# Optimization experiments

Hardware: AMD Instinct MI355X
Metric: run time of the kernel (lower is better)

Reference implementation:

```python
import jax, jax.numpy as jnp
import numpy as np

T, B, I, H = 128, 128, 256, 256  # numHiddenUnits(=seq len), batch, input_size, hidden_size


def setup_inputs() -> dict:
    key = jax.random.key(0)
    ks = jax.random.split(key, 7)
    stdv = 1.0 / np.sqrt(H)
    u = lambda k, shape: jax.random.uniform(k, shape, jnp.float32, -stdv, stdv)
    return {
        "batch_x": jax.random.normal(ks[0], (T, B, I), jnp.float32),
        "initial_state": jax.random.normal(ks[1], (B, H), jnp.float32),
        "initial_state_c": jax.random.normal(ks[2], (B, H), jnp.float32),
        # distinct weights per timestep (one LSTMCell per t), stacked on dim 0
        "W_input": u(ks[3], (T, I, 4 * H)),
        "B_input": u(ks[4], (T, 4 * H)),
        "W_hidden": u(ks[5], (T, H, 4 * H)),
        "B_hidden": u(ks[6], (T, 4 * H)),
    }


def reference(batch_x, initial_state, initial_state_c, W_input, B_input, W_hidden, B_hidden):
    def step(carry, xs):
        h, c = carry
        x_t, Wi, bi, Wh, bh = xs
        gates = x_t @ Wi + bi + h @ Wh + bh  # [B, 4H]
        i_t, f_t, o_t, g_t = jnp.split(gates, 4, axis=1)  # chunk order: i, f, o, c_tilde
        c = jax.nn.sigmoid(f_t) * c + jax.nn.sigmoid(i_t) * jnp.tanh(g_t)
        h = jax.nn.sigmoid(o_t) * jnp.tanh(c)
        return (h, c), h

    (h, c), outputs = jax.lax.scan(
        step, (initial_state, initial_state_c),
        (batch_x, W_input, B_input, W_hidden, B_hidden))
    return outputs, h, c  # outputs: [T, B, H]
```

## Files before the change

### kernel.cpp

```cpp
#include <hip/hip_runtime.h>
#include <hip/hip_bf16.h>
#include <cmath>

#define T_  128
#define B_  128
#define I_  256
#define H_  256
#define G4_ 1024

#define NP1 512
#define NRP 8192

using frag  = __attribute__((ext_vector_type(8))) short;
using f32x4 = __attribute__((ext_vector_type(4))) float;
using u32x4 = __attribute__((ext_vector_type(4))) unsigned int;

__device__ __forceinline__ unsigned short bf16u(float f) {
    __hip_bfloat16 b = __float2bfloat16(f);
    return __builtin_bit_cast(unsigned short, b);
}

#define BARRIER_SEQ() do {                                   \
    __builtin_amdgcn_sched_barrier(0);                       \
    asm volatile("s_waitcnt lgkmcnt(0)" ::: "memory");       \
    __builtin_amdgcn_s_barrier();                            \
    __builtin_amdgcn_sched_barrier(0);                       \
} while (0)

__global__ __launch_bounds__(512)
void lstm_pre(const float* __restrict__ x, const float* __restrict__ Wi,
              const float* __restrict__ bi, const float* __restrict__ bh,
              const float* __restrict__ Wh,
              float* __restrict__ Gxp, unsigned short* __restrict__ Whp)
{
    const int bid = blockIdx.x;
    const int tid = threadIdx.x;

    if (bid >= NP1) {
        const int pbid = bid - NP1;
        const int tt   = pbid >> 6;
        const int j64  = pbid & 63;
        const int gid  = tt * 32768 + j64 * 512 + tid;
        const int lane = gid & 63;
        const int nb   = (gid >> 6) & 63;
        const int kb   = (gid >> 12) & 7;
        const int k0   = kb * 32 + (lane >> 4) * 8;
        const int col  = nb * 16 + (lane & 15);
        const float* src = Wh + (size_t)(tt * I_ + k0) * G4_ + col;
        unsigned short v[8];
        #pragma unroll
        for (int j = 0; j < 8; ++j) v[j] = bf16u(src[(size_t)j * G4_]);
        uint4 o;
        o.x = v[0] | ((unsigned)v[1] << 16);
        o.y = v[2] | ((unsigned)v[3] << 16);
        o.z = v[4] | ((unsigned)v[5] << 16);
        o.w = v[6] | ((unsigned)v[7] << 16);
        *(uint4*)(Whp + (size_t)gid * 8) = o;
        return;
    }

    __shared__ unsigned short ws[2][16][64][8];

    const int t    = bid >> 2;
    const int q    = bid & 3;
    const int wv   = tid >> 6;
    const int lane = tid & 63;
    const int lrow = lane & 15;
    const int lhi  = lane >> 4;

    frag af[8];
    #pragma unroll
    for (int kb = 0; kb < 8; ++kb) {
        const float* ap = x + ((size_t)(t * B_ + wv * 16 + lrow) * I_ + kb * 32 + lhi * 8);
        float4 f0 = *(const float4*)ap;
        float4 f1 = *(const float4*)(ap + 4);
        u32x4 p;
        p.x = bf16u(f0.x) | ((unsigned)bf16u(f0.y) << 16);
        p.y = bf16u(f0.z) | ((unsigned)bf16u(f0.w) << 16);
        p.z = bf16u(f1.x) | ((unsigned)bf16u(f1.y) << 16);
        p.w = bf16u(f1.z) | ((unsigned)bf16u(f1.w) << 16);
        af[kb] = __builtin_bit_cast(frag, p);
    }

    f32x4 acc[16];
    #pragma unroll
    for (int n = 0; n < 16; ++n) {
        const int gc = (q * 16 + n) * 16 + lrow;
        const float b = bi[(size_t)t * G4_ + gc] + bh[(size_t)t * G4_ + gc];
        acc[n] = (f32x4){b, b, b, b};
    }

    auto stage = [&](int kb, int b) {
        #pragma unroll
        for (int p = 0; p < 2; ++p) {
            const int task = p * 512 + tid;
            const int colL = task & 255;
            const int khi  = task >> 8;
            const float* src = Wi + ((size_t)(t * I_ + kb * 32 + khi * 8) * G4_
                                     + q * 256 + colL);
            unsigned short v[8];
            #pragma unroll
            for (int j = 0; j < 8; ++j) v[j] = bf16u(src[(size_t)j * G4_]);
            uint4 o;
            o.x = v[0] | ((unsigned)v[1] << 16);
            o.y = v[2] | ((unsigned)v[3] << 16);
            o.z = v[4] | ((unsigned)v[5] << 16);
            o.w = v[6] | ((unsigned)v[7] << 16);
            const int nbh = colL >> 4;
            const int lw  = (colL & 15) | (khi << 4);
            *(uint4*)&ws[b][nbh][lw][0] = o;
        }
    };

    stage(0, 0);
    __syncthreads();
    for (int kb = 0; kb < 8; ++kb) {
        if (kb < 7) stage(kb + 1, (kb + 1) & 1);
        #pragma unroll
        for (int n = 0; n < 16; ++n) {
            frag bf = *(const frag*)&ws[kb & 1][n][lane][0];
            acc[n] = __builtin_amdgcn_mfma_f32_16x16x32_bf16(af[kb], bf, acc[n], 0, 0, 0);
        }
        __syncthreads();
    }

    #pragma unroll
    for (int n = 0; n < 16; ++n)
        *(f32x4*)&Gxp[(((size_t)t * 8 + wv) * 64 + q * 16 + n) * 256 + lane * 4] = acc[n];
}

__global__ __launch_bounds__(512, 1)
void lstm_rec(const float* __restrict__ h0, const float* __restrict__ c0in,
              const unsigned short* __restrict__ Whp,
              const float* __restrict__ Gxp, float* __restrict__ out,
              unsigned int* __restrict__ pub)
{
    __shared__ unsigned short h2[2][16][272];
    __shared__ float red[4][4][256];

    const int tid  = threadIdx.x;
    const int wv   = tid >> 6;
    const int lane = tid & 63;
    const int rg   = blockIdx.x & 7;
    const int sl   = blockIdx.x >> 3;
    const int r0   = rg * 16;
    const int oc0  = sl * 64;
    const int lrow = lane & 15;
    const int lhi  = lane >> 4;

    const int kh = wv >> 2;
    const int cb = wv & 3;

    {
        int row = tid >> 5;
        int cc  = (tid & 31) * 8;
        #pragma unroll
        for (int j = 0; j < 8; ++j)
            h2[0][row][cc + j] = bf16u(h0[(size_t)(r0 + row) * H_ + cc + j]);
    }

    float cst[4] = {0.f, 0.f, 0.f, 0.f};
    if (kh == 0) {
        #pragma unroll
        for (int rgi = 0; rgi < 4; ++rgi)
            cst[rgi] = c0in[(size_t)(r0 + lhi * 4 + rgi) * H_ + oc0 + cb * 16 + lrow];
    }

    int prow[12], pcol[12];
    if (kh == 1) {
        const int ltid = tid - 256;
        #pragma unroll
        for (int k = 0; k < 12; ++k) {
            int w  = ltid + k * 256;
            int rr = w / 192;
            int fc = w - rr * 192;
            prow[k] = rr;
            pcol[k] = fc + (fc >= oc0 ? 64 : 0);
        }
    }

    const unsigned short* wl = Whp + (size_t)lane * 8;
    const float*          gl = Gxp + (size_t)lane * 4;

    frag br[4][4];
    #pragma unroll
    for (int kbl = 0; kbl < 4; ++kbl)
        #pragma unroll
        for (int g = 0; g < 4; ++g)
            br[kbl][g] = *(const frag*)(wl +
                (size_t)((kh * 4 + kbl) * 64 + g * 16 + sl * 4 + cb) * 512);

    f32x4 gxr[4];
    if (kh == 0) {
        #pragma unroll
        for (int g = 0; g < 4; ++g)
            gxr[g] = *(const f32x4*)(gl +
                (size_t)((size_t)rg * 64 + g * 16 + sl * 4 + cb) * 256);
    }

    __syncthreads();

    for (int t = 0; t < T_; ++t) {
        f32x4 acc[4];
        if (kh == 0) {
            #pragma unroll
            for (int g = 0; g < 4; ++g) acc[g] = gxr[g];
            if (t + 1 < T_) {
                #pragma unroll
                for (int g = 0; g < 4; ++g)
                    gxr[g] = *(const f32x4*)(gl +
                        (size_t)(((t + 1) * 8 + rg) * 64 + g * 16 + sl * 4 + cb) * 256);
            }
        } else {
            #pragma unroll
            for (int g = 0; g < 4; ++g) acc[g] = (f32x4){0.f, 0.f, 0.f, 0.f};
        }

        #pragma unroll
        for (int kbl = 0; kbl < 4; ++kbl) {
            const int kb = kh * 4 + kbl;
            frag a = *(const frag*)&h2[t & 1][lrow][kb * 32 + lhi * 8];
            #pragma unroll
            for (int g = 0; g < 4; ++g)
                acc[g] = __builtin_amdgcn_mfma_f32_16x16x32_bf16(
                    a, br[kbl][g], acc[g], 0, 0, 0);
            if (t + 1 < T_) {
                #pragma unroll
                for (int g = 0; g < 4; ++g)
                    br[kbl][g] = *(const frag*)(wl +
                        (size_t)(((t + 1) * 8 + kb) * 64 + g * 16 + sl * 4 + cb) * 512);
            }
        }

        if (kh == 1) {
            #pragma unroll
            for (int g = 0; g < 4; ++g)
                *(f32x4*)&red[cb][g][lane * 4] = acc[g];
        }

        BARRIER_SEQ();

        if (kh == 0) {
            #pragma unroll
            for (int g = 0; g < 4; ++g)
                acc[g] += *(const f32x4*)&red[cb][g][lane * 4];
            const int colb = oc0 + cb * 16 + lrow;
            float hv[4];
            unsigned short hb[4];
            #pragma unroll
            for (int rgi = 0; rgi < 4; ++rgi) {
                float gi = acc[0][rgi], gf = acc[1][rgi];
                float go = acc[2][rgi], gg = acc[3][rgi];
                float i_ = __builtin_amdgcn_rcpf(1.f + __expf(-gi));
                float f_ = __builtin_amdgcn_rcpf(1.f + __expf(-gf));
                float o_ = __builtin_amdgcn_rcpf(1.f + __expf(-go));
                float gt = 1.f - 2.f * __builtin_amdgcn_rcpf(__expf(2.f * gg) + 1.f);
                float c  = f_ * cst[rgi] + i_ * gt;
                cst[rgi] = c;
                float tc = 1.f - 2.f * __builtin_amdgcn_rcpf(__expf(2.f * c) + 1.f);
                float h  = o_ * tc;
                hv[rgi] = h;
                hb[rgi] = bf16u(h);
            }
            if (t + 1 < T_) {
                #pragma unroll
                for (int rgi = 0; rgi < 4; ++rgi)
                    __hip_atomic_store(&pub[(size_t)(r0 + lhi * 4 + rgi) * H_ + colb],
                                       ((unsigned)(t + 1) << 16) | hb[rgi],
                                       __ATOMIC_RELAXED, __HIP_MEMORY_SCOPE_AGENT);
            }
            #pragma unroll
            for (int rgi = 0; rgi < 4; ++rgi) {
                const int row = lhi * 4 + rgi;
                out[(size_t)(t * B_ + r0 + row) * H_ + colb] = hv[rgi];
                h2[(t + 1) & 1][row][colb] = hb[rgi];
            }
            if (t == T_ - 1) {
                #pragma unroll
                for (int rgi = 0; rgi < 4; ++rgi) {
                    const int row = lhi * 4 + rgi;
                    out[(size_t)T_ * B_ * H_ + (size_t)(r0 + row) * H_ + colb] = hv[rgi];
                    out[(size_t)T_ * B_ * H_ + B_ * H_ + (size_t)(r0 + row) * H_ + colb] = cst[rgi];
                }
            }
        } else if (t + 1 < T_) {
            const unsigned want = (unsigned)(t + 1);
            while (true) {
                unsigned vv[12];
                #pragma unroll
                for (int k = 0; k < 12; ++k)
                    vv[k] = __hip_atomic_load(
                        &pub[(size_t)(r0 + prow[k]) * H_ + pcol[k]],
                        __ATOMIC_RELAXED, __HIP_MEMORY_SCOPE_AGENT);
                unsigned miss = 0;
                #pragma unroll
                for (int k = 0; k < 12; ++k) {
                    if ((vv[k] >> 16) == want)
                        h2[(t + 1) & 1][prow[k]][pcol[k]] =
                            (unsigned short)(vv[k] & 0xFFFFu);
                    else
                        miss = 1u;
                }
                if (!__any((int)miss)) break;
            }
        }

        BARRIER_SEQ();
    }
}

extern "C" void kernel_launch(void* const* d_in, const int* in_sizes, int n_in,
                              void* d_out, int out_size, void* d_ws, size_t ws_size,
                              hipStream_t stream) {
    const float* x  = (const float*)d_in[0];
    const float* h0 = (const float*)d_in[1];
    const float* c0 = (const float*)d_in[2];
    const float* Wi = (const float*)d_in[3];
    const float* bi = (const float*)d_in[4];
    const float* Wh = (const float*)d_in[5];
    const float* bh = (const float*)d_in[6];
    float* out = (float*)d_out;

    float*          Gxp = (float*)d_ws;
    unsigned short* Whp = (unsigned short*)((char*)d_ws + 67108864);
    unsigned int*   pub = (unsigned int*)((char*)d_ws + 134217728);

    hipMemsetAsync(pub, 0, 131072, stream);
    lstm_pre<<<dim3(NP1 + NRP), dim3(512), 0, stream>>>(x, Wi, bi, bh, Wh, Gxp, Whp);
    lstm_rec<<<dim3(32), dim3(512), 0, stream>>>(h0, c0, Whp, Gxp, out, pub);
}
```

Baseline: 485.8 us.

## Split LSTM gate epilogue and peer polling across both K-half wave groups

Both K-half wave groups now write partial gate sums to shared memory. Each group reduces and computes the LSTM cell update for two of the four rows per lane, instead of one group doing all four while the other only polls. Polling of peer-published hidden values is also split evenly across all 512 threads, and the first poll load is issued before the gate math so its latency overlaps the compute. The aim is to shorten the serial epilogue and cross-block sync on the recurrent critical path, at the cost of more LDS traffic for the reduction buffer.

After: 507.7 us. +4.5%, slower.

```diff
diff --git a/kernel.cpp b/kernel.cpp
--- a/kernel.cpp
+++ b/kernel.cpp
@@ -42,8 +42,8 @@
         const int j64  = pbid & 63;
         const int gid  = tt * 32768 + j64 * 512 + tid;
         const int lane = gid & 63;
+        const int kb   = (gid >> 12) & 7;
         const int nb   = (gid >> 6) & 63;
-        const int kb   = (gid >> 12) & 7;
         const int k0   = kb * 32 + (lane >> 4) * 8;
         const int col  = nb * 16 + (lane & 15);
         const float* src = Wh + (size_t)(tt * I_ + k0) * G4_ + col;
@@ -136,7 +136,7 @@
               unsigned int* __restrict__ pub)
 {
     __shared__ unsigned short h2[2][16][272];
-    __shared__ float red[4][4][256];
+    __shared__ float red[2][4][4][256];
 
     const int tid  = threadIdx.x;
     const int wv   = tid >> 6;
@@ -159,24 +159,20 @@
             h2[0][row][cc + j] = bf16u(h0[(size_t)(r0 + row) * H_ + cc + j]);
     }
 
-    float cst[4] = {0.f, 0.f, 0.f, 0.f};
-    if (kh == 0) {
-        #pragma unroll
-        for (int rgi = 0; rgi < 4; ++rgi)
-            cst[rgi] = c0in[(size_t)(r0 + lhi * 4 + rgi) * H_ + oc0 + cb * 16 + lrow];
-    }
-
-    int prow[12], pcol[12];
-    if (kh == 1) {
-        const int ltid = tid - 256;
-        #pragma unroll
-        for (int k = 0; k < 12; ++k) {
-            int w  = ltid + k * 256;
-            int rr = w / 192;
-            int fc = w - rr * 192;
-            prow[k] = rr;
-            pcol[k] = fc + (fc >= oc0 ? 64 : 0);
-        }
+    const int colb = oc0 + cb * 16 + lrow;
+    float cst[2];
+    #pragma unroll
+    for (int j = 0; j < 2; ++j)
+        cst[j] = c0in[(size_t)(r0 + lhi * 4 + kh * 2 + j) * H_ + colb];
+
+    int prow[6], pcol[6];
+    #pragma unroll
+    for (int k = 0; k < 6; ++k) {
+        int w  = tid + k * 512;
+        int rr = w / 192;
+        int fc = w - rr * 192;
+        prow[k] = rr;
+        pcol[k] = fc + (fc >= oc0 ? 64 : 0);
     }
 
     const unsigned short* wl = Whp + (size_t)lane * 8;
@@ -232,69 +228,77 @@
             }
         }
 
-        if (kh == 1) {
-            #pragma unroll
-            for (int g = 0; g < 4; ++g)
-                *(f32x4*)&red[cb][g][lane * 4] = acc[g];
-        }
+        #pragma unroll
+        for (int g = 0; g < 4; ++g)
+            *(f32x4*)&red[kh][cb][g][lane * 4] = acc[g];
 
         BARRIER_SEQ();
 
-        if (kh == 0) {
-            #pragma unroll
-            for (int g = 0; g < 4; ++g)
-                acc[g] += *(const f32x4*)&red[cb][g][lane * 4];
-            const int colb = oc0 + cb * 16 + lrow;
-            float hv[4];
-            unsigned short hb[4];
-            #pragma unroll
-            for (int rgi = 0; rgi < 4; ++rgi) {
-                float gi = acc[0][rgi], gf = acc[1][rgi];
-                float go = acc[2][rgi], gg = acc[3][rgi];
-                float i_ = __builtin_amdgcn_rcpf(1.f + __expf(-gi));
-                float f_ = __builtin_amdgcn_rcpf(1.f + __expf(-gf));
-                float o_ = __builtin_amdgcn_rcpf(1.f + __expf(-go));
-                float gt = 1.f - 2.f * __builtin_amdgcn_rcpf(__expf(2.f * gg) + 1.f);
-                float c  = f_ * cst[rgi] + i_ * gt;
-                cst[rgi] = c;
-                float tc = 1.f - 2.f * __builtin_amdgcn_rcpf(__expf(2.f * c) + 1.f);
-                float h  = o_ * tc;
-                hv[rgi] = h;
-                hb[rgi] = bf16u(h);
-            }
-            if (t + 1 < T_) {
-                #pragma unroll
-                for (int rgi = 0; rgi < 4; ++rgi)
-                    __hip_atomic_store(&pub[(size_t)(r0 + lhi * 4 + rgi) * H_ + colb],
-                                       ((unsigned)(t + 1) << 16) | hb[rgi],
-                                       __ATOMIC_RELAXED, __HIP_MEMORY_SCOPE_AGENT);
-            }
-            #pragma unroll
-            for (int rgi = 0; rgi < 4; ++rgi) {
-                const int row = lhi * 4 + rgi;
-                out[(size_t)(t * B_ + r0 + row) * H_ + colb] = hv[rgi];
-                h2[(t + 1) & 1][row][colb] = hb[rgi];
-            }
-            if (t == T_ - 1) {
-                #pragma unroll
-                for (int rgi = 0; rgi < 4; ++rgi) {
-                    const int row = lhi * 4 + rgi;
-                    out[(size_t)T_ * B_ * H_ + (size_t)(r0 + row) * H_ + colb] = hv[rgi];
-                    out[(size_t)T_ * B_ * H_ + B_ * H_ + (size_t)(r0 + row) * H_ + colb] = cst[rgi];
-                }
-            }
-        } else if (t + 1 < T_) {
-            const unsigned want = (unsigned)(t + 1);
+        unsigned vv[6];
+        const unsigned want = (unsigned)(t + 1);
+        if (t + 1 < T_) {
+            #pragma unroll
+            for (int k = 0; k < 6; ++k)
+                vv[k] = __hip_atomic_load(
+                    &pub[(size_t)(r0 + prow[k]) * H_ + pcol[k]],
+                    __ATOMIC_RELAXED, __HIP_MEMORY_SCOPE_AGENT);
+        }
+
+        float gate[4][2];
+        #pragma unroll
+        for (int g = 0; g < 4; ++g) {
+            f32x4 a0 = *(const f32x4*)&red[0][cb][g][lane * 4];
+            f32x4 a1 = *(const f32x4*)&red[1][cb][g][lane * 4];
+            if (kh == 0) {
+                gate[g][0] = a0[0] + a1[0];
+                gate[g][1] = a0[1] + a1[1];
+            } else {
+                gate[g][0] = a0[2] + a1[2];
+                gate[g][1] = a0[3] + a1[3];
+            }
+        }
+        float hv[2];
+        unsigned short hb[2];
+        #pragma unroll
+        for (int j = 0; j < 2; ++j) {
+            float i_ = __builtin_amdgcn_rcpf(1.f + __expf(-gate[0][j]));
+            float f_ = __builtin_amdgcn_rcpf(1.f + __expf(-gate[1][j]));
+            float o_ = __builtin_amdgcn_rcpf(1.f + __expf(-gate[2][j]));
+            float gt = 1.f - 2.f * __builtin_amdgcn_rcpf(__expf(2.f * gate[3][j]) + 1.f);
+            float c  = f_ * cst[j] + i_ * gt;
+            cst[j] = c;
+            float tc = 1.f - 2.f * __builtin_amdgcn_rcpf(__expf(2.f * c) + 1.f);
+            hv[j] = o_ * tc;
+            hb[j] = bf16u(hv[j]);
+        }
+        if (t + 1 < T_) {
+            #pragma unroll
+            for (int j = 0; j < 2; ++j)
+                __hip_atomic_store(
+                    &pub[(size_t)(r0 + lhi * 4 + kh * 2 + j) * H_ + colb],
+                    (want << 16) | hb[j],
+                    __ATOMIC_RELAXED, __HIP_MEMORY_SCOPE_AGENT);
+        }
+        #pragma unroll
+        for (int j = 0; j < 2; ++j) {
+            const int row = lhi * 4 + kh * 2 + j;
+            out[(size_t)(t * B_ + r0 + row) * H_ + colb] = hv[j];
+            h2[(t + 1) & 1][row][colb] = hb[j];
+        }
+        if (t == T_ - 1) {
+            #pragma unroll
+            for (int j = 0; j < 2; ++j) {
+                const int row = lhi * 4 + kh * 2 + j;
+                out[(size_t)T_ * B_ * H_ + (size_t)(r0 + row) * H_ + colb] = hv[j];
+                out[(size_t)T_ * B_ * H_ + B_ * H_ + (size_t)(r0 + row) * H_ + colb] = cst[j];
+            }
+        }
+
+        if (t + 1 < T_) {
             while (true) {
-                unsigned vv[12];
-                #pragma unroll
-                for (int k = 0; k < 12; ++k)
-                    vv[k] = __hip_atomic_load(
-                        &pub[(size_t)(r0 + prow[k]) * H_ + pcol[k]],
-                        __ATOMIC_RELAXED, __HIP_MEMORY_SCOPE_AGENT);
                 unsigned miss = 0;
                 #pragma unroll
-                for (int k = 0; k < 12; ++k) {
+                for (int k = 0; k < 6; ++k) {
                     if ((vv[k] >> 16) == want)
                         h2[(t + 1) & 1][prow[k]][pcol[k]] =
                             (unsigned short)(vv[k] & 0xFFFFu);
@@ -302,6 +306,11 @@
                         miss = 1u;
                 }
                 if (!__any((int)miss)) break;
+                #pragma unroll
+                for (int k = 0; k < 6; ++k)
+                    vv[k] = __hip_atomic_load(
+                        &pub[(size_t)(r0 + prow[k]) * H_ + pcol[k]],
+                        __ATOMIC_RELAXED, __HIP_MEMORY_SCOPE_AGENT);
             }
         }
 
```

## Specialize waves: compute waves do full K, poller waves only gather h

Applied to the files above, without the earlier changes.

Restructures the recurrent kernel so the four compute waves run the whole K=256 reduction themselves, with a rotating weight-register prefetch. This removes the split-K LDS reduction and the extra barrier wait between the two wave halves. The other four waves become dedicated pollers that only gather the published h values, and the compute waves raise their scheduling priority. The trade-off is that each compute wave now does twice the MFMA work per step, so the serial chain per timestep gets longer.

New measurement: 706.9 us. 1.46x slower.

```diff
diff --git a/kernel.cpp b/kernel.cpp
--- a/kernel.cpp
+++ b/kernel.cpp
@@ -42,8 +42,8 @@
         const int j64  = pbid & 63;
         const int gid  = tt * 32768 + j64 * 512 + tid;
         const int lane = gid & 63;
+        const int kb   = (gid >> 12) & 7;
         const int nb   = (gid >> 6) & 63;
-        const int kb   = (gid >> 12) & 7;
         const int k0   = kb * 32 + (lane >> 4) * 8;
         const int col  = nb * 16 + (lane & 15);
         const float* src = Wh + (size_t)(tt * I_ + k0) * G4_ + col;
@@ -136,7 +136,6 @@
               unsigned int* __restrict__ pub)
 {
     __shared__ unsigned short h2[2][16][272];
-    __shared__ float red[4][4][256];
 
     const int tid  = threadIdx.x;
     const int wv   = tid >> 6;
@@ -148,9 +147,6 @@
     const int lrow = lane & 15;
     const int lhi  = lane >> 4;
 
-    const int kh = wv >> 2;
-    const int cb = wv & 3;
-
     {
         int row = tid >> 5;
         int cc  = (tid & 31) * 8;
@@ -158,51 +154,37 @@
         for (int j = 0; j < 8; ++j)
             h2[0][row][cc + j] = bf16u(h0[(size_t)(r0 + row) * H_ + cc + j]);
     }
-
-    float cst[4] = {0.f, 0.f, 0.f, 0.f};
-    if (kh == 0) {
+    __syncthreads();
+
+    if (wv < 4) {
+        __builtin_amdgcn_s_setprio(1);
+        const int cb   = wv;
+        const int colb = oc0 + cb * 16 + lrow;
+
+        float cst[4];
         #pragma unroll
         for (int rgi = 0; rgi < 4; ++rgi)
-            cst[rgi] = c0in[(size_t)(r0 + lhi * 4 + rgi) * H_ + oc0 + cb * 16 + lrow];
-    }
-
-    int prow[12], pcol[12];
-    if (kh == 1) {
-        const int ltid = tid - 256;
-        #pragma unroll
-        for (int k = 0; k < 12; ++k) {
-            int w  = ltid + k * 256;
-            int rr = w / 192;
-            int fc = w - rr * 192;
-            prow[k] = rr;
-            pcol[k] = fc + (fc >= oc0 ? 64 : 0);
-        }
-    }
-
-    const unsigned short* wl = Whp + (size_t)lane * 8;
-    const float*          gl = Gxp + (size_t)lane * 4;
-
-    frag br[4][4];
-    #pragma unroll
-    for (int kbl = 0; kbl < 4; ++kbl)
-        #pragma unroll
-        for (int g = 0; g < 4; ++g)
-            br[kbl][g] = *(const frag*)(wl +
-                (size_t)((kh * 4 + kbl) * 64 + g * 16 + sl * 4 + cb) * 512);
-
-    f32x4 gxr[4];
-    if (kh == 0) {
+            cst[rgi] = c0in[(size_t)(r0 + lhi * 4 + rgi) * H_ + colb];
+
+        const unsigned short* wl = Whp + (size_t)lane * 8;
+        const float*          gl = Gxp + (size_t)lane * 4;
+
+        frag br[4][4];
+        #pragma unroll
+        for (int c = 0; c < 4; ++c)
+            #pragma unroll
+            for (int g = 0; g < 4; ++g)
+                br[c][g] = *(const frag*)(wl +
+                    (size_t)(c * 64 + g * 16 + sl * 4 + cb) * 512);
+
+        f32x4 gxr[4];
         #pragma unroll
         for (int g = 0; g < 4; ++g)
             gxr[g] = *(const f32x4*)(gl +
                 (size_t)((size_t)rg * 64 + g * 16 + sl * 4 + cb) * 256);
-    }
-
-    __syncthreads();
-
-    for (int t = 0; t < T_; ++t) {
-        f32x4 acc[4];
-        if (kh == 0) {
+
+        for (int t = 0; t < T_; ++t) {
+            f32x4 acc[4];
             #pragma unroll
             for (int g = 0; g < 4; ++g) acc[g] = gxr[g];
             if (t + 1 < T_) {
@@ -211,56 +193,37 @@
                     gxr[g] = *(const f32x4*)(gl +
                         (size_t)(((t + 1) * 8 + rg) * 64 + g * 16 + sl * 4 + cb) * 256);
             }
-        } else {
-            #pragma unroll
-            for (int g = 0; g < 4; ++g) acc[g] = (f32x4){0.f, 0.f, 0.f, 0.f};
-        }
-
-        #pragma unroll
-        for (int kbl = 0; kbl < 4; ++kbl) {
-            const int kb = kh * 4 + kbl;
-            frag a = *(const frag*)&h2[t & 1][lrow][kb * 32 + lhi * 8];
-            #pragma unroll
-            for (int g = 0; g < 4; ++g)
-                acc[g] = __builtin_amdgcn_mfma_f32_16x16x32_bf16(
-                    a, br[kbl][g], acc[g], 0, 0, 0);
-            if (t + 1 < T_) {
+
+            #pragma unroll
+            for (int kb = 0; kb < 8; ++kb) {
+                frag a = *(const frag*)&h2[t & 1][lrow][kb * 32 + lhi * 8];
                 #pragma unroll
                 for (int g = 0; g < 4; ++g)
-                    br[kbl][g] = *(const frag*)(wl +
-                        (size_t)(((t + 1) * 8 + kb) * 64 + g * 16 + sl * 4 + cb) * 512);
-            }
-        }
-
-        if (kh == 1) {
-            #pragma unroll
-            for (int g = 0; g < 4; ++g)
-                *(f32x4*)&red[cb][g][lane * 4] = acc[g];
-        }
-
-        BARRIER_SEQ();
-
-        if (kh == 0) {
-            #pragma unroll
-            for (int g = 0; g < 4; ++g)
-                acc[g] += *(const f32x4*)&red[cb][g][lane * 4];
-            const int colb = oc0 + cb * 16 + lrow;
+                    acc[g] = __builtin_amdgcn_mfma_f32_16x16x32_bf16(
+                        a, br[kb & 3][g], acc[g], 0, 0, 0);
+                const int tn = (kb < 4) ? t : t + 1;
+                const int kn = (kb < 4) ? kb + 4 : kb - 4;
+                if (tn < T_) {
+                    #pragma unroll
+                    for (int g = 0; g < 4; ++g)
+                        br[kb & 3][g] = *(const frag*)(wl +
+                            (size_t)((tn * 8 + kn) * 64 + g * 16 + sl * 4 + cb) * 512);
+                }
+            }
+
             float hv[4];
             unsigned short hb[4];
             #pragma unroll
             for (int rgi = 0; rgi < 4; ++rgi) {
-                float gi = acc[0][rgi], gf = acc[1][rgi];
-                float go = acc[2][rgi], gg = acc[3][rgi];
-                float i_ = __builtin_amdgcn_rcpf(1.f + __expf(-gi));
-                float f_ = __builtin_amdgcn_rcpf(1.f + __expf(-gf));
-                float o_ = __builtin_amdgcn_rcpf(1.f + __expf(-go));
-                float gt = 1.f - 2.f * __builtin_amdgcn_rcpf(__expf(2.f * gg) + 1.f);
+                float i_ = __builtin_amdgcn_rcpf(1.f + __expf(-acc[0][rgi]));
+                float f_ = __builtin_amdgcn_rcpf(1.f + __expf(-acc[1][rgi]));
+                float o_ = __builtin_amdgcn_rcpf(1.f + __expf(-acc[2][rgi]));
+                float gt = 1.f - 2.f * __builtin_amdgcn_rcpf(__expf(2.f * acc[3][rgi]) + 1.f);
                 float c  = f_ * cst[rgi] + i_ * gt;
                 cst[rgi] = c;
                 float tc = 1.f - 2.f * __builtin_amdgcn_rcpf(__expf(2.f * c) + 1.f);
-                float h  = o_ * tc;
-                hv[rgi] = h;
-                hb[rgi] = bf16u(h);
+                hv[rgi] = o_ * tc;
+                hb[rgi] = bf16u(hv[rgi]);
             }
             if (t + 1 < T_) {
                 #pragma unroll
@@ -283,29 +246,46 @@
                     out[(size_t)T_ * B_ * H_ + B_ * H_ + (size_t)(r0 + row) * H_ + colb] = cst[rgi];
                 }
             }
-        } else if (t + 1 < T_) {
-            const unsigned want = (unsigned)(t + 1);
-            while (true) {
-                unsigned vv[12];
-                #pragma unroll
-                for (int k = 0; k < 12; ++k)
-                    vv[k] = __hip_atomic_load(
-                        &pub[(size_t)(r0 + prow[k]) * H_ + pcol[k]],
-                        __ATOMIC_RELAXED, __HIP_MEMORY_SCOPE_AGENT);
-                unsigned miss = 0;
-                #pragma unroll
-                for (int k = 0; k < 12; ++k) {
-                    if ((vv[k] >> 16) == want)
-                        h2[(t + 1) & 1][prow[k]][pcol[k]] =
-                            (unsigned short)(vv[k] & 0xFFFFu);
-                    else
-                        miss = 1u;
+
+            BARRIER_SEQ();
+        }
+    } else {
+        const int ltid = tid - 256;
+        int prow[12], pcol[12];
+        #pragma unroll
+        for (int k = 0; k < 12; ++k) {
+            int w  = ltid + k * 256;
+            int rr = w / 192;
+            int fc = w - rr * 192;
+            prow[k] = rr;
+            pcol[k] = fc + (fc >= oc0 ? 64 : 0);
+        }
+
+        for (int t = 0; t < T_; ++t) {
+            if (t + 1 < T_) {
+                const unsigned want = (unsigned)(t + 1);
+                while (true) {
+                    unsigned vv[12];
+                    #pragma unroll
+                    for (int k = 0; k < 12; ++k)
+                        vv[k] = __hip_atomic_load(
+                            &pub[(size_t)(r0 + prow[k]) * H_ + pcol[k]],
+                            __ATOMIC_RELAXED, __HIP_MEMORY_SCOPE_AGENT);
+                    unsigned miss = 0;
+                    #pragma unroll
+                    for (int k = 0; k < 12; ++k) {
+                        if ((vv[k] >> 16) == want)
+                            h2[(t + 1) & 1][prow[k]][pcol[k]] =
+                                (unsigned short)(vv[k] & 0xFFFFu);
+                        else
+                            miss = 1u;
+                    }
+                    if (!__any((int)miss)) break;
                 }
-                if (!__any((int)miss)) break;
-            }
-        }
-
-        BARRIER_SEQ();
+            }
+
+            BARRIER_SEQ();
+        }
     }
 }
 
```
